# Kernel tuning notes

Measured on AMD Instinct MI355X. Metric: run time of the kernel, lower is better.

## Reference

```python
import jax, jax.numpy as jnp
import numpy as np

B, T, D, K = 8, 2048, 384, 64

def setup_inputs() -> dict:
    key = jax.random.key(0)
    k1, k2, k3, k4 = jax.random.split(key, 4)
    x = jax.random.normal(k1, (B, T, D), dtype=jnp.float32)
    # torch nn.Linear default init scale ~ 1/sqrt(fan_in); use scaled normals
    Wq = jax.random.normal(k2, (D, K), dtype=jnp.float32) / np.sqrt(D)
    Wk = jax.random.normal(k3, (D, K), dtype=jnp.float32) / np.sqrt(D)
    Wv = jax.random.normal(k4, (D, D), dtype=jnp.float32) / np.sqrt(D)
    return {"x": x, "Wq": Wq, "Wk": Wk, "Wv": Wv}

def reference(x, Wq, Wk, Wv):
    # x: (B,T,D)
    q = jnp.einsum('btd,dk->btk', x, Wq)      # (B,T,K)
    k = jnp.einsum('btd,dk->btk', x, Wk)      # (B,T,K)
    v = jnp.einsum('btd,de->bte', x, Wv)      # (B,T,D)
    scores = jnp.einsum('bqk,bsk->bqs', q, k) / jnp.sqrt(jnp.float32(K))  # (B,T,T)
    causal = jnp.tril(jnp.ones((T, T), dtype=bool))
    scores = jnp.where(causal, scores, -jnp.inf)
    weights = jax.nn.softmax(scores, axis=-1)
    out = jnp.einsum('bqs,bse->bqe', weights, v)  # (B,T,D)
    return out
```

## Files before the change

### kernel.cpp

```cpp
#include <hip/hip_runtime.h>

#define TT 2048
#define DD 384

typedef float f32x4 __attribute__((ext_vector_type(4)));
typedef float f32x16 __attribute__((ext_vector_type(16)));
typedef short s16x8 __attribute__((ext_vector_type(8)));
typedef unsigned int u32x4 __attribute__((ext_vector_type(4)));

static __device__ __forceinline__ unsigned short f2bf(float f) {
    unsigned int u = __builtin_bit_cast(unsigned int, f);
    u = (u + 0x7fffu + ((u >> 16) & 1u)) >> 16;
    return (unsigned short)u;
}
static __device__ __forceinline__ unsigned int pk2(float a, float b) {
    unsigned int ua = __builtin_bit_cast(unsigned int, a);
    unsigned int ub = __builtin_bit_cast(unsigned int, b);
    ua = (ua + 0x7fffu + ((ua >> 16) & 1u)) >> 16;
    ub = (ub + 0x7fffu + ((ub >> 16) & 1u)) & 0xffff0000u;
    return ua | ub;
}

__global__ __launch_bounds__(256, 2) void qkv_gemm(
    const float* __restrict__ x, const float* __restrict__ Wq,
    const float* __restrict__ Wk, const float* __restrict__ Wv,
    unsigned short* __restrict__ qo, unsigned short* __restrict__ ko,
    unsigned short* __restrict__ vto)
{
    __shared__ __align__(16) unsigned short lds[16384];
    const int tid = threadIdx.x;
    const int l   = tid & 63;
    const int w   = tid >> 6;
    const int si  = l & 15;
    const int qq  = l >> 4;
    const int m0  = blockIdx.x * 128;
    const int nb  = blockIdx.y;
    const int wr  = w >> 1, wc = w & 1;

    const int bn = tid & 127;
    const int bk = (tid >> 7) * 16;
    const float* wsrc; int ldw;
    if (nb == 0) { wsrc = (bn < 64) ? (Wq + bn) : (Wk + (bn - 64)); ldw = 64; }
    else         { wsrc = Wv + (nb - 1) * 128 + bn;                 ldw = 384; }

    f32x4 acc[4][4];
    #pragma unroll
    for (int rt = 0; rt < 4; ++rt)
        #pragma unroll
        for (int ct = 0; ct < 4; ++ct) acc[rt][ct] = (f32x4){0.f, 0.f, 0.f, 0.f};

    for (int kt = 0; kt < 12; ++kt) {
        const int k0 = kt * 32;
        #pragma unroll
        for (int i = 0; i < 2; ++i) {
            const int u = tid + 256 * i, r = u >> 2, c = u & 3;
            const float* xp = x + (size_t)(m0 + r) * DD + k0 + c * 8;
            f32x4 x0 = *(const f32x4*)xp;
            f32x4 x1 = *(const f32x4*)(xp + 4);
            s16x8 av;
            av[0] = (short)f2bf(x0[0]); av[1] = (short)f2bf(x0[1]);
            av[2] = (short)f2bf(x0[2]); av[3] = (short)f2bf(x0[3]);
            av[4] = (short)f2bf(x1[0]); av[5] = (short)f2bf(x1[1]);
            av[6] = (short)f2bf(x1[2]); av[7] = (short)f2bf(x1[3]);
            *(s16x8*)&lds[r * 32 + ((c ^ (r & 3)) * 8)] = av;
        }
        {
            float t[16];
            #pragma unroll
            for (int j = 0; j < 16; ++j) t[j] = wsrc[(size_t)(k0 + bk + j) * ldw];
            #pragma unroll
            for (int jj = 0; jj < 2; ++jj) {
                s16x8 bv;
                #pragma unroll
                for (int j = 0; j < 8; ++j) bv[j] = (short)f2bf(t[jj * 8 + j]);
                const int ch = (tid >> 7) * 2 + jj;
                *(s16x8*)&lds[4096 + bn * 32 + ((ch ^ (bn & 3)) * 8)] = bv;
            }
        }
        __syncthreads();

        s16x8 af[4], bf[4];
        #pragma unroll
        for (int rt = 0; rt < 4; ++rt) {
            const int row = wr * 64 + rt * 16 + si;
            af[rt] = *(const s16x8*)&lds[row * 32 + ((qq ^ (row & 3)) * 8)];
        }
        #pragma unroll
        for (int ct = 0; ct < 4; ++ct) {
            const int col = wc * 64 + ct * 16 + si;
            bf[ct] = *(const s16x8*)&lds[4096 + col * 32 + ((qq ^ (col & 3)) * 8)];
        }
        #pragma unroll
        for (int rt = 0; rt < 4; ++rt)
            #pragma unroll
            for (int ct = 0; ct < 4; ++ct)
                acc[rt][ct] = __builtin_amdgcn_mfma_f32_16x16x32_bf16(af[rt], bf[ct], acc[rt][ct], 0, 0, 0);
        __syncthreads();
    }

    if (nb == 0) {
        unsigned short* dst = (wc == 0) ? qo : ko;
        const float sc = (wc == 0) ? 0.125f : 1.0f;
        #pragma unroll
        for (int rt = 0; rt < 4; ++rt)
            #pragma unroll
            for (int ct = 0; ct < 4; ++ct)
                #pragma unroll
                for (int r = 0; r < 4; ++r) {
                    const int m = m0 + wr * 64 + rt * 16 + qq * 4 + r;
                    dst[(size_t)m * 64 + ct * 16 + si] = f2bf(acc[rt][ct][r] * sc);
                }
    } else {
        #pragma unroll
        for (int rt = 0; rt < 4; ++rt)
            #pragma unroll
            for (int ct = 0; ct < 4; ++ct)
                #pragma unroll
                for (int r = 0; r < 4; ++r) {
                    const int m = wr * 64 + rt * 16 + qq * 4 + r;
                    const int n = wc * 64 + ct * 16 + si;
                    lds[n * 128 + (((m >> 3) ^ (n & 7)) * 8) + (m & 7)] = f2bf(acc[rt][ct][r]);
                }
        __syncthreads();
        const int bbat = m0 >> 11, t0 = m0 & 2047;
        #pragma unroll
        for (int i = 0; i < 8; ++i) {
            const int u = tid + 256 * i, n = u >> 4, mc = u & 15;
            s16x8 v = *(const s16x8*)&lds[n * 128 + ((mc ^ (n & 7)) * 8)];
            *(s16x8*)&vto[((size_t)bbat * DD + ((nb - 1) * 128 + n)) * TT + t0 + mc * 8] = v;
        }
    }
}

__global__ __launch_bounds__(512, 4) void attn(
    const unsigned short* __restrict__ qg, const unsigned short* __restrict__ kg,
    const unsigned short* __restrict__ vg, float* __restrict__ out)
{
    __shared__ __align__(16) unsigned short lds[20480];
    __shared__ float stL[256];

    const int tid = threadIdx.x;
    const int l   = tid & 63;
    const int w   = tid >> 6;
    const int par = w >> 2;
    const int qb  = w & 3;
    const int lo  = l & 31;
    const int hi  = l >> 5;

    const int g  = blockIdx.x;
    const int bb = g & 7;
    const int eq = (g >> 3) & 3;
    const int jidx = g >> 5;
    const int j  = (g < 256) ? jidx : (23 - jidx);
    const int q0 = j * 128;
    const int e0 = eq * 96;
    const int qrow = q0 + qb * 32 + lo;

    s16x8 qf[4];
    {
        const unsigned short* qp = qg + ((size_t)bb * TT + qrow) * 64;
        #pragma unroll
        for (int st = 0; st < 4; ++st) qf[st] = *(const s16x8*)(qp + st * 16 + hi * 8);
    }

    f32x16 o[3];
    #pragma unroll
    for (int et = 0; et < 3; ++et)
        #pragma unroll
        for (int r = 0; r < 16; ++r) o[et][r] = 0.f;
    float lp = 0.f;

    unsigned short* Ks = lds + par * 4096;
    unsigned short* Vs = lds + 8192 + par * 6144;

    for (int it = 0; it <= j; ++it) {
        #pragma unroll
        for (int i = 0; i < 2; ++i) {
            const int u = tid + 512 * i;
            const int p = u >> 9, r = (u >> 3) & 63, c = u & 7;
            s16x8 v = *(const s16x8*)(kg + ((size_t)bb * TT + (2 * it + p) * 64 + r) * 64 + c * 8);
            *(s16x8*)&lds[p * 4096 + r * 64 + ((c ^ (r & 7)) * 8)] = v;
        }
        #pragma unroll
        for (int i = 0; i < 3; ++i) {
            const int u = tid + 512 * i;
            const int p = (u >= 768) ? 1 : 0;
            const int idx = u - 768 * p;
            const int r = idx >> 3, c = idx & 7;
            s16x8 v = *(const s16x8*)(vg + ((size_t)bb * DD + e0 + r) * TT + (2 * it + p) * 64 + c * 8);
            *(s16x8*)&lds[8192 + p * 6144 + r * 64 + ((c ^ (r & 7)) * 8)] = v;
        }
        __syncthreads();

        const int s0 = (2 * it + par) * 64;
        if (s0 <= q0 + qb * 32 + 31) {
            const bool mb = (s0 + 63 > q0 + qb * 32);
            #pragma unroll
            for (int ct = 0; ct < 2; ++ct) {
                f32x16 sa;
                #pragma unroll
                for (int r = 0; r < 16; ++r) sa[r] = 0.f;
                #pragma unroll
                for (int st = 0; st < 4; ++st) {
                    s16x8 kf = *(const s16x8*)&Ks[(ct * 32 + lo) * 64 + (((st * 2 + hi) ^ (lo & 7)) * 8)];
                    sa = __builtin_amdgcn_mfma_f32_32x32x16_bf16(kf, qf[st], sa, 0, 0, 0);
                }
                float pv[16];
                #pragma unroll
                for (int r = 0; r < 16; ++r) {
                    float e = __expf(sa[r]);
                    if (mb) {
                        const int srow = s0 + ct * 32 + (r & 3) + 8 * (r >> 2) + 4 * hi;
                        if (srow > qrow) e = 0.f;
                    }
                    pv[r] = e;
                    lp += e;
                }
                unsigned int d0 = pk2(pv[0], pv[1]),   d1 = pk2(pv[2], pv[3]);
                unsigned int d2 = pk2(pv[4], pv[5]),   d3 = pk2(pv[6], pv[7]);
                unsigned int d4 = pk2(pv[8], pv[9]),   d5 = pk2(pv[10], pv[11]);
                unsigned int d6 = pk2(pv[12], pv[13]), d7 = pk2(pv[14], pv[15]);
                unsigned int sA0 = hi ? d0 : d2, sA1 = hi ? d1 : d3;
                unsigned int rA0 = (unsigned int)__shfl_xor((int)sA0, 32);
                unsigned int rA1 = (unsigned int)__shfl_xor((int)sA1, 32);
                u32x4 fa0 = hi ? (u32x4){rA0, rA1, d2, d3} : (u32x4){d0, d1, rA0, rA1};
                unsigned int sB0 = hi ? d4 : d6, sB1 = hi ? d5 : d7;
                unsigned int rB0 = (unsigned int)__shfl_xor((int)sB0, 32);
                unsigned int rB1 = (unsigned int)__shfl_xor((int)sB1, 32);
                u32x4 fa1 = hi ? (u32x4){rB0, rB1, d6, d7} : (u32x4){d4, d5, rB0, rB1};
                s16x8 a0 = __builtin_bit_cast(s16x8, fa0);
                s16x8 a1 = __builtin_bit_cast(s16x8, fa1);
                #pragma unroll
                for (int et = 0; et < 3; ++et) {
                    const int el = et * 32 + lo;
                    s16x8 v0 = *(const s16x8*)&Vs[el * 64 + (((ct * 4 + hi) ^ (el & 7)) * 8)];
                    o[et] = __builtin_amdgcn_mfma_f32_32x32x16_bf16(a0, v0, o[et], 0, 0, 0);
                    s16x8 v1 = *(const s16x8*)&Vs[el * 64 + (((ct * 4 + 2 + hi) ^ (el & 7)) * 8)];
                    o[et] = __builtin_amdgcn_mfma_f32_32x32x16_bf16(a1, v1, o[et], 0, 0, 0);
                }
            }
        }
        __syncthreads();
    }

    lp += __shfl_xor(lp, 32);
    if (hi == 0) stL[par * 128 + qb * 32 + lo] = lp;
    __syncthreads();

    float* fb = (float*)lds;
    #pragma unroll
    for (int ph = 0; ph < 2; ++ph) {
        if (par == 1 && (qb >> 1) == ph) {
            const int slot = qb & 1;
            #pragma unroll
            for (int r = 0; r < 16; ++r) {
                const int rloc = (r & 3) + 8 * (r >> 2) + 4 * hi;
                #pragma unroll
                for (int et = 0; et < 3; ++et)
                    fb[slot * 3072 + rloc * 96 + et * 32 + lo] = o[et][r];
            }
        }
        __syncthreads();
        if (par == 0 && (qb >> 1) == ph) {
            const int slot = qb & 1;
            #pragma unroll
            for (int r = 0; r < 16; ++r) {
                const int rloc = (r & 3) + 8 * (r >> 2) + 4 * hi;
                const float linv = 1.f / (stL[qb * 32 + rloc] + stL[128 + qb * 32 + rloc]);
                float* op = out + ((size_t)bb * TT + q0 + qb * 32 + rloc) * DD + e0;
                #pragma unroll
                for (int et = 0; et < 3; ++et)
                    op[et * 32 + lo] = (o[et][r] + fb[slot * 3072 + rloc * 96 + et * 32 + lo]) * linv;
            }
        }
        __syncthreads();
    }
}

extern "C" void kernel_launch(void* const* d_in, const int* in_sizes, int n_in,
                              void* d_out, int out_size, void* d_ws, size_t ws_size,
                              hipStream_t stream)
{
    const float* x  = (const float*)d_in[0];
    const float* Wq = (const float*)d_in[1];
    const float* Wk = (const float*)d_in[2];
    const float* Wv = (const float*)d_in[3];

    unsigned short* qws  = (unsigned short*)d_ws;
    unsigned short* kws  = (unsigned short*)((char*)d_ws + ((size_t)2 << 20));
    unsigned short* vtws = (unsigned short*)((char*)d_ws + ((size_t)4 << 20));

    qkv_gemm<<<dim3(128, 4), dim3(256), 0, stream>>>(x, Wq, Wk, Wv, qws, kws, vtws);
    attn<<<dim3(512), dim3(512), 0, stream>>>(qws, kws, vtws, (float*)d_out);
}
```

Before: 147.6 us.

## Split attention output dim into six 64-wide slices with balanced block schedule

```diff
diff --git a/kernel.cpp b/kernel.cpp
--- a/kernel.cpp
+++ b/kernel.cpp
@@ -20,6 +20,13 @@
     ub = (ub + 0x7fffu + ((ub >> 16) & 1u)) & 0xffff0000u;
     return ua | ub;
 }
+
+__device__ __constant__ unsigned char Tj[16][3] = {
+    {15,7,0},{15,6,2},{15,4,3},{14,8,0},{14,5,4},{14,6,3},{13,9,0},{13,8,1},
+    {13,7,3},{12,9,1},{12,10,1},{12,6,4},{11,9,2},{11,10,2},{11,7,5},{10,8,5}};
+__device__ __constant__ unsigned char EQA[16][3] = {
+    {0,0,0},{1,0,0},{2,0,0},{0,0,1},{1,0,1},{2,1,1},{0,0,2},{1,1,0},
+    {2,1,2},{0,1,1},{1,0,2},{2,2,2},{0,2,1},{1,1,2},{2,2,1},{2,2,2}};
 
 __global__ __launch_bounds__(256, 2) void qkv_gemm(
     const float* __restrict__ x, const float* __restrict__ Wq,
@@ -132,11 +139,11 @@
     }
 }
 
-__global__ __launch_bounds__(512, 4) void attn(
+__global__ __launch_bounds__(512, 6) void attn(
     const unsigned short* __restrict__ qg, const unsigned short* __restrict__ kg,
     const unsigned short* __restrict__ vg, float* __restrict__ out)
 {
-    __shared__ __align__(16) unsigned short lds[20480];
+    __shared__ __align__(16) unsigned short lds[16384];
     __shared__ float stL[256];
 
     const int tid = threadIdx.x;
@@ -149,11 +156,12 @@
 
     const int g  = blockIdx.x;
     const int bb = g & 7;
-    const int eq = (g >> 3) & 3;
-    const int jidx = g >> 5;
-    const int j  = (g < 256) ? jidx : (23 - jidx);
+    const int u  = g >> 3;
+    const int vr = u & 31, tp = u >> 5;
+    const int j  = Tj[vr & 15][tp];
+    const int eq = 2 * EQA[vr & 15][tp] + (vr >> 4);
     const int q0 = j * 128;
-    const int e0 = eq * 96;
+    const int e0 = eq * 64;
     const int qrow = q0 + qb * 32 + lo;
 
     s16x8 qf[4];
@@ -163,32 +171,30 @@
         for (int st = 0; st < 4; ++st) qf[st] = *(const s16x8*)(qp + st * 16 + hi * 8);
     }
 
-    f32x16 o[3];
+    f32x16 o[2];
     #pragma unroll
-    for (int et = 0; et < 3; ++et)
+    for (int et = 0; et < 2; ++et)
         #pragma unroll
         for (int r = 0; r < 16; ++r) o[et][r] = 0.f;
     float lp = 0.f;
 
     unsigned short* Ks = lds + par * 4096;
-    unsigned short* Vs = lds + 8192 + par * 6144;
+    unsigned short* Vs = lds + 8192 + par * 4096;
 
     for (int it = 0; it <= j; ++it) {
         #pragma unroll
         for (int i = 0; i < 2; ++i) {
-            const int u = tid + 512 * i;
-            const int p = u >> 9, r = (u >> 3) & 63, c = u & 7;
+            const int u2 = tid + 512 * i;
+            const int p = u2 >> 9, r = (u2 >> 3) & 63, c = u2 & 7;
             s16x8 v = *(const s16x8*)(kg + ((size_t)bb * TT + (2 * it + p) * 64 + r) * 64 + c * 8);
             *(s16x8*)&lds[p * 4096 + r * 64 + ((c ^ (r & 7)) * 8)] = v;
         }
         #pragma unroll
-        for (int i = 0; i < 3; ++i) {
-            const int u = tid + 512 * i;
-            const int p = (u >= 768) ? 1 : 0;
-            const int idx = u - 768 * p;
-            const int r = idx >> 3, c = idx & 7;
+        for (int i = 0; i < 2; ++i) {
+            const int u2 = tid + 512 * i;
+            const int p = u2 >> 9, r = (u2 >> 3) & 63, c = u2 & 7;
             s16x8 v = *(const s16x8*)(vg + ((size_t)bb * DD + e0 + r) * TT + (2 * it + p) * 64 + c * 8);
-            *(s16x8*)&lds[8192 + p * 6144 + r * 64 + ((c ^ (r & 7)) * 8)] = v;
+            *(s16x8*)&lds[8192 + p * 4096 + r * 64 + ((c ^ (r & 7)) * 8)] = v;
         }
         __syncthreads();
 
@@ -205,7 +211,6 @@
                     s16x8 kf = *(const s16x8*)&Ks[(ct * 32 + lo) * 64 + (((st * 2 + hi) ^ (lo & 7)) * 8)];
                     sa = __builtin_amdgcn_mfma_f32_32x32x16_bf16(kf, qf[st], sa, 0, 0, 0);
                 }
-                float pv[16];
                 #pragma unroll
                 for (int r = 0; r < 16; ++r) {
                     float e = __expf(sa[r]);
@@ -213,13 +218,13 @@
                         const int srow = s0 + ct * 32 + (r & 3) + 8 * (r >> 2) + 4 * hi;
                         if (srow > qrow) e = 0.f;
                     }
-                    pv[r] = e;
+                    sa[r] = e;
                     lp += e;
                 }
-                unsigned int d0 = pk2(pv[0], pv[1]),   d1 = pk2(pv[2], pv[3]);
-                unsigned int d2 = pk2(pv[4], pv[5]),   d3 = pk2(pv[6], pv[7]);
-                unsigned int d4 = pk2(pv[8], pv[9]),   d5 = pk2(pv[10], pv[11]);
-                unsigned int d6 = pk2(pv[12], pv[13]), d7 = pk2(pv[14], pv[15]);
+                unsigned int d0 = pk2(sa[0], sa[1]),   d1 = pk2(sa[2], sa[3]);
+                unsigned int d2 = pk2(sa[4], sa[5]),   d3 = pk2(sa[6], sa[7]);
+                unsigned int d4 = pk2(sa[8], sa[9]),   d5 = pk2(sa[10], sa[11]);
+                unsigned int d6 = pk2(sa[12], sa[13]), d7 = pk2(sa[14], sa[15]);
                 unsigned int sA0 = hi ? d0 : d2, sA1 = hi ? d1 : d3;
                 unsigned int rA0 = (unsigned int)__shfl_xor((int)sA0, 32);
                 unsigned int rA1 = (unsigned int)__shfl_xor((int)sA1, 32);
@@ -231,7 +236,7 @@
                 s16x8 a0 = __builtin_bit_cast(s16x8, fa0);
                 s16x8 a1 = __builtin_bit_cast(s16x8, fa1);
                 #pragma unroll
-                for (int et = 0; et < 3; ++et) {
+                for (int et = 0; et < 2; ++et) {
                     const int el = et * 32 + lo;
                     s16x8 v0 = *(const s16x8*)&Vs[el * 64 + (((ct * 4 + hi) ^ (el & 7)) * 8)];
                     o[et] = __builtin_amdgcn_mfma_f32_32x32x16_bf16(a0, v0, o[et], 0, 0, 0);
@@ -245,35 +250,28 @@
 
     lp += __shfl_xor(lp, 32);
     if (hi == 0) stL[par * 128 + qb * 32 + lo] = lp;
+
+    float* fb = (float*)lds;
+    if (par == 1) {
+        #pragma unroll
+        for (int r = 0; r < 16; ++r) {
+            const int rloc = (r & 3) + 8 * (r >> 2) + 4 * hi;
+            #pragma unroll
+            for (int et = 0; et < 2; ++et)
+                fb[qb * 2048 + rloc * 64 + et * 32 + lo] = o[et][r];
+        }
+    }
     __syncthreads();
-
-    float* fb = (float*)lds;
-    #pragma unroll
-    for (int ph = 0; ph < 2; ++ph) {
-        if (par == 1 && (qb >> 1) == ph) {
-            const int slot = qb & 1;
-            #pragma unroll
-            for (int r = 0; r < 16; ++r) {
-                const int rloc = (r & 3) + 8 * (r >> 2) + 4 * hi;
-                #pragma unroll
-                for (int et = 0; et < 3; ++et)
-                    fb[slot * 3072 + rloc * 96 + et * 32 + lo] = o[et][r];
-            }
-        }
-        __syncthreads();
-        if (par == 0 && (qb >> 1) == ph) {
-            const int slot = qb & 1;
-            #pragma unroll
-            for (int r = 0; r < 16; ++r) {
-                const int rloc = (r & 3) + 8 * (r >> 2) + 4 * hi;
-                const float linv = 1.f / (stL[qb * 32 + rloc] + stL[128 + qb * 32 + rloc]);
-                float* op = out + ((size_t)bb * TT + q0 + qb * 32 + rloc) * DD + e0;
-                #pragma unroll
-                for (int et = 0; et < 3; ++et)
-                    op[et * 32 + lo] = (o[et][r] + fb[slot * 3072 + rloc * 96 + et * 32 + lo]) * linv;
-            }
-        }
-        __syncthreads();
+    if (par == 0) {
+        #pragma unroll
+        for (int r = 0; r < 16; ++r) {
+            const int rloc = (r & 3) + 8 * (r >> 2) + 4 * hi;
+            const float linv = 1.f / (stL[qb * 32 + rloc] + stL[128 + qb * 32 + rloc]);
+            float* op = out + ((size_t)bb * TT + q0 + qb * 32 + rloc) * DD + e0;
+            #pragma unroll
+            for (int et = 0; et < 2; ++et)
+                op[et * 32 + lo] = (o[et][r] + fb[qb * 2048 + rloc * 64 + et * 32 + lo]) * linv;
+        }
     }
 }
 
@@ -291,5 +289,5 @@
     unsigned short* vtws = (unsigned short*)((char*)d_ws + ((size_t)4 << 20));
 
     qkv_gemm<<<dim3(128, 4), dim3(256), 0, stream>>>(x, Wq, Wk, Wv, qws, kws, vtws);
-    attn<<<dim3(512), dim3(512), 0, stream>>>(qws, kws, vtws, (float*)d_out);
-}
+    attn<<<dim3(768), dim3(512), 0, stream>>>(qws, kws, vtws, (float*)d_out);
+}
```

Measured after the change: 200.8 us. 1.36x slower.

## Prefetch next K/V tiles into registers and use hardware bf16 pack conversion

Applied to the files above, without the earlier changes.

```diff
diff --git a/kernel.cpp b/kernel.cpp
--- a/kernel.cpp
+++ b/kernel.cpp
@@ -6,6 +6,7 @@
 typedef float f32x4 __attribute__((ext_vector_type(4)));
 typedef float f32x16 __attribute__((ext_vector_type(16)));
 typedef short s16x8 __attribute__((ext_vector_type(8)));
+typedef short s16x2 __attribute__((ext_vector_type(2)));
 typedef unsigned int u32x4 __attribute__((ext_vector_type(4)));
 
 static __device__ __forceinline__ unsigned short f2bf(float f) {
@@ -14,11 +15,16 @@
     return (unsigned short)u;
 }
 static __device__ __forceinline__ unsigned int pk2(float a, float b) {
+#if __has_builtin(__builtin_amdgcn_cvt_pk_bf16_f32)
+    s16x2 t = __builtin_amdgcn_cvt_pk_bf16_f32(a, b);
+    return __builtin_bit_cast(unsigned int, t);
+#else
     unsigned int ua = __builtin_bit_cast(unsigned int, a);
     unsigned int ub = __builtin_bit_cast(unsigned int, b);
     ua = (ua + 0x7fffu + ((ua >> 16) & 1u)) >> 16;
     ub = (ub + 0x7fffu + ((ub >> 16) & 1u)) & 0xffff0000u;
     return ua | ub;
+#endif
 }
 
 __global__ __launch_bounds__(256, 2) void qkv_gemm(
@@ -173,24 +179,45 @@
     unsigned short* Ks = lds + par * 4096;
     unsigned short* Vs = lds + 8192 + par * 6144;
 
+    const int kr = (tid >> 3) & 63, kc = tid & 7;
+    const unsigned short* ksrc0 = kg + ((size_t)bb * TT + kr) * 64 + kc * 8;
+    const unsigned short* ksrc1 = ksrc0 + 64 * 64;
+    const int kd0 = kr * 64 + ((kc ^ (kr & 7)) * 8);
+    const int kd1 = 4096 + kd0;
+    int vrr[3], vdd[3];
+    const unsigned short* vsrc[3];
+    #pragma unroll
+    for (int i = 0; i < 3; ++i) {
+        const int u2 = tid + 512 * i;
+        const int p = (u2 >= 768) ? 1 : 0;
+        const int idx = u2 - 768 * p;
+        const int r = idx >> 3, c = idx & 7;
+        vsrc[i] = vg + ((size_t)bb * DD + e0 + r) * TT + p * 64 + c * 8;
+        vdd[i]  = 8192 + p * 6144 + r * 64 + ((c ^ (r & 7)) * 8);
+        vrr[i]  = r;
+    }
+
+    s16x8 kpre0 = *(const s16x8*)ksrc0;
+    s16x8 kpre1 = *(const s16x8*)ksrc1;
+    s16x8 vpre[3];
+    #pragma unroll
+    for (int i = 0; i < 3; ++i) vpre[i] = *(const s16x8*)vsrc[i];
+
     for (int it = 0; it <= j; ++it) {
-        #pragma unroll
-        for (int i = 0; i < 2; ++i) {
-            const int u = tid + 512 * i;
-            const int p = u >> 9, r = (u >> 3) & 63, c = u & 7;
-            s16x8 v = *(const s16x8*)(kg + ((size_t)bb * TT + (2 * it + p) * 64 + r) * 64 + c * 8);
-            *(s16x8*)&lds[p * 4096 + r * 64 + ((c ^ (r & 7)) * 8)] = v;
-        }
-        #pragma unroll
-        for (int i = 0; i < 3; ++i) {
-            const int u = tid + 512 * i;
-            const int p = (u >= 768) ? 1 : 0;
-            const int idx = u - 768 * p;
-            const int r = idx >> 3, c = idx & 7;
-            s16x8 v = *(const s16x8*)(vg + ((size_t)bb * DD + e0 + r) * TT + (2 * it + p) * 64 + c * 8);
-            *(s16x8*)&lds[8192 + p * 6144 + r * 64 + ((c ^ (r & 7)) * 8)] = v;
-        }
-        __syncthreads();
+        *(s16x8*)&lds[kd0] = kpre0;
+        *(s16x8*)&lds[kd1] = kpre1;
+        #pragma unroll
+        for (int i = 0; i < 3; ++i) *(s16x8*)&lds[vdd[i]] = vpre[i];
+        __syncthreads();
+
+        if (it < j) {
+            const size_t kof = (size_t)(it + 1) * 8192;
+            kpre0 = *(const s16x8*)(ksrc0 + kof);
+            kpre1 = *(const s16x8*)(ksrc1 + kof);
+            const int vof = (it + 1) * 128;
+            #pragma unroll
+            for (int i = 0; i < 3; ++i) vpre[i] = *(const s16x8*)(vsrc[i] + vof);
+        }
 
         const int s0 = (2 * it + par) * 64;
         if (s0 <= q0 + qb * 32 + 31) {
```

Measured after the change: 178.6 us. 21.0% more time.

## Double-buffer K/V tiles with async global-to-LDS loads in attention

Applied to the files above, without the earlier changes.

```diff
diff --git a/kernel.cpp b/kernel.cpp
--- a/kernel.cpp
+++ b/kernel.cpp
@@ -6,7 +6,12 @@
 typedef float f32x4 __attribute__((ext_vector_type(4)));
 typedef float f32x16 __attribute__((ext_vector_type(16)));
 typedef short s16x8 __attribute__((ext_vector_type(8)));
+typedef short s16x2 __attribute__((ext_vector_type(2)));
 typedef unsigned int u32x4 __attribute__((ext_vector_type(4)));
+
+typedef __attribute__((address_space(3))) unsigned char* as3p;
+typedef const __attribute__((address_space(1))) unsigned char* as1p;
+#define GLLDS(gsrc, ldst) __builtin_amdgcn_global_load_lds((as1p)(gsrc), (as3p)(ldst), 16, 0, 0)
 
 static __device__ __forceinline__ unsigned short f2bf(float f) {
     unsigned int u = __builtin_bit_cast(unsigned int, f);
@@ -14,11 +19,16 @@
     return (unsigned short)u;
 }
 static __device__ __forceinline__ unsigned int pk2(float a, float b) {
+#if __has_builtin(__builtin_amdgcn_cvt_pk_bf16_f32)
+    s16x2 t = __builtin_amdgcn_cvt_pk_bf16_f32(a, b);
+    return __builtin_bit_cast(unsigned int, t);
+#else
     unsigned int ua = __builtin_bit_cast(unsigned int, a);
     unsigned int ub = __builtin_bit_cast(unsigned int, b);
     ua = (ua + 0x7fffu + ((ua >> 16) & 1u)) >> 16;
     ub = (ub + 0x7fffu + ((ub >> 16) & 1u)) & 0xffff0000u;
     return ua | ub;
+#endif
 }
 
 __global__ __launch_bounds__(256, 2) void qkv_gemm(
@@ -99,17 +109,28 @@
     }
 
     if (nb == 0) {
-        unsigned short* dst = (wc == 0) ? qo : ko;
-        const float sc = (wc == 0) ? 0.125f : 1.0f;
-        #pragma unroll
-        for (int rt = 0; rt < 4; ++rt)
-            #pragma unroll
-            for (int ct = 0; ct < 4; ++ct)
-                #pragma unroll
-                for (int r = 0; r < 4; ++r) {
-                    const int m = m0 + wr * 64 + rt * 16 + qq * 4 + r;
-                    dst[(size_t)m * 64 + ct * 16 + si] = f2bf(acc[rt][ct][r] * sc);
-                }
+        if (wc == 0) {
+            #pragma unroll
+            for (int rt = 0; rt < 4; ++rt)
+                #pragma unroll
+                for (int ct = 0; ct < 4; ++ct)
+                    #pragma unroll
+                    for (int r = 0; r < 4; ++r) {
+                        const int m = m0 + wr * 64 + rt * 16 + qq * 4 + r;
+                        qo[(size_t)m * 64 + ct * 16 + si] = f2bf(acc[rt][ct][r] * 0.125f);
+                    }
+        } else {
+            #pragma unroll
+            for (int rt = 0; rt < 4; ++rt)
+                #pragma unroll
+                for (int ct = 0; ct < 4; ++ct)
+                    #pragma unroll
+                    for (int r = 0; r < 4; ++r) {
+                        const int m = m0 + wr * 64 + rt * 16 + qq * 4 + r;
+                        const int col = ct * 16 + si;
+                        ko[(size_t)m * 64 + (((col >> 3) ^ (m & 7)) * 8) + (col & 7)] = f2bf(acc[rt][ct][r]);
+                    }
+        }
     } else {
         #pragma unroll
         for (int rt = 0; rt < 4; ++rt)
@@ -127,7 +148,8 @@
         for (int i = 0; i < 8; ++i) {
             const int u = tid + 256 * i, n = u >> 4, mc = u & 15;
             s16x8 v = *(const s16x8*)&lds[n * 128 + ((mc ^ (n & 7)) * 8)];
-            *(s16x8*)&vto[((size_t)bbat * DD + ((nb - 1) * 128 + n)) * TT + t0 + mc * 8] = v;
+            *(s16x8*)&vto[((size_t)bbat * DD + ((nb - 1) * 128 + n)) * TT
+                          + t0 + (mc >> 3) * 64 + (((mc & 7) ^ (n & 7)) * 8)] = v;
         }
     }
 }
@@ -136,8 +158,7 @@
     const unsigned short* __restrict__ qg, const unsigned short* __restrict__ kg,
     const unsigned short* __restrict__ vg, float* __restrict__ out)
 {
-    __shared__ __align__(16) unsigned short lds[20480];
-    __shared__ float stL[256];
+    __shared__ __align__(16) unsigned short lds[40960];
 
     const int tid = threadIdx.x;
     const int l   = tid & 63;
@@ -170,27 +191,36 @@
         for (int r = 0; r < 16; ++r) o[et][r] = 0.f;
     float lp = 0.f;
 
-    unsigned short* Ks = lds + par * 4096;
-    unsigned short* Vs = lds + 8192 + par * 6144;
+    const unsigned short* kbase = kg + (size_t)bb * TT * 64;
+    const unsigned short* vbase = vg + ((size_t)bb * DD + e0) * TT;
+
+    #define STAGE(IT, BUF)                                                                  \
+    {                                                                                       \
+        const unsigned short* kb = kbase + (size_t)(IT) * 128 * 64;                         \
+        unsigned short* kl = &lds[(BUF) * 8192];                                            \
+        GLLDS(kb + (2 * w) * 512 + l * 8,     &kl[(2 * w) * 512]);                          \
+        GLLDS(kb + (2 * w + 1) * 512 + l * 8, &kl[(2 * w + 1) * 512]);                      \
+        unsigned short* vl = &lds[16384 + (BUF) * 12288];                                   \
+        _Pragma("unroll")                                                                   \
+        for (int c3 = 0; c3 < 3; ++c3) {                                                    \
+            const int ch = 3 * w + c3;                                                      \
+            const int p = ch / 12, rr = (ch % 12) * 8;                                      \
+            const unsigned short* vb = vbase + ((size_t)(rr + (l >> 3))) * TT               \
+                                       + (IT) * 128 + p * 64 + (l & 7) * 8;                 \
+            GLLDS(vb, &vl[ch * 512]);                                                       \
+        }                                                                                   \
+    }
+
+    STAGE(0, 0);
 
     for (int it = 0; it <= j; ++it) {
-        #pragma unroll
-        for (int i = 0; i < 2; ++i) {
-            const int u = tid + 512 * i;
-            const int p = u >> 9, r = (u >> 3) & 63, c = u & 7;
-            s16x8 v = *(const s16x8*)(kg + ((size_t)bb * TT + (2 * it + p) * 64 + r) * 64 + c * 8);
-            *(s16x8*)&lds[p * 4096 + r * 64 + ((c ^ (r & 7)) * 8)] = v;
-        }
-        #pragma unroll
-        for (int i = 0; i < 3; ++i) {
-            const int u = tid + 512 * i;
-            const int p = (u >= 768) ? 1 : 0;
-            const int idx = u - 768 * p;
-            const int r = idx >> 3, c = idx & 7;
-            s16x8 v = *(const s16x8*)(vg + ((size_t)bb * DD + e0 + r) * TT + (2 * it + p) * 64 + c * 8);
-            *(s16x8*)&lds[8192 + p * 6144 + r * 64 + ((c ^ (r & 7)) * 8)] = v;
-        }
-        __syncthreads();
+        const int buf = it & 1;
+        __syncthreads();
+
+        if (it < j) STAGE(it + 1, 1 - buf);
+
+        const unsigned short* Ks = &lds[buf * 8192 + par * 4096];
+        const unsigned short* Vs = &lds[16384 + buf * 12288 + par * 6144];
 
         const int s0 = (2 * it + par) * 64;
         if (s0 <= q0 + qb * 32 + 31) {
@@ -240,14 +270,15 @@
                 }
             }
         }
-        __syncthreads();
-    }
-
+    }
+    __syncthreads();
+
+    float* fb  = (float*)lds;
+    float* stL = (float*)lds + 6144;
     lp += __shfl_xor(lp, 32);
     if (hi == 0) stL[par * 128 + qb * 32 + lo] = lp;
     __syncthreads();
 
-    float* fb = (float*)lds;
     #pragma unroll
     for (int ph = 0; ph < 2; ++ph) {
         if (par == 1 && (qb >> 1) == ph) {
```

Measured after the change: 143.4 us. 2.8% less time.
